# Kernel tuning notes

Hardware: AMD Instinct MI355X
Metric: run time of the kernel (lower is better)

## Reference

```python
import jax, jax.numpy as jnp
import numpy as np


def _conv(x, w, stride, dil):
    # VALID conv in NCHW / OIHW layout with rhs (kernel) dilation
    return jax.lax.conv_general_dilated(
        x, w, window_strides=stride, padding='VALID', rhs_dilation=dil,
        dimension_numbers=('NCHW', 'OIHW', 'NCHW'))


def setup_inputs() -> dict:
    key = jax.random.key(0)
    k1, k2, k3 = jax.random.split(key, 3)
    B, Cin, H, W = 8, 64, 256, 256  # W even => columns_mod2 == 0
    Cout = 128
    inp = jax.random.normal(k1, (B, Cin, H, W), dtype=jnp.float32)
    # kaiming-normal-style init as in the torch module
    fan0 = Cin * 3 * 1
    kernel0 = jax.random.normal(k2, (Cout, Cin, 3, 1), dtype=jnp.float32) * np.float32(np.sqrt(2.0 / fan0))
    fan1 = Cin * 2 * 2
    kernel1 = jax.random.normal(k3, (Cout, Cin, 2, 2), dtype=jnp.float32) * np.float32(np.sqrt(2.0 / fan1))
    bias = jnp.full((Cout,), 0.01, dtype=jnp.float32)
    return {'input': inp, 'kernel0': kernel0, 'kernel1': kernel1, 'bias': bias}


def reference(input, kernel0, kernel1, bias):
    # hexagdly conv2d, size=1, stride=1, even number of columns (columns_mod2 = 0)
    x = input
    # kernel0: vertical 3x1 stencil over all columns; bias added once here
    even_all = _conv(jnp.pad(x, ((0, 0), (0, 0), (1, 1), (0, 0))), kernel0, (1, 1), (1, 1))
    even_all = even_all + bias[None, :, None, None]
    # kernel1: 2x2 stencil with horizontal dilation 2, stride 2 in width,
    # with column-parity-dependent vertical offset (hex grid)
    # odd columns: ZeroPad2d(left=1, right=0, top=1, bottom=0)
    ooc = _conv(jnp.pad(x, ((0, 0), (0, 0), (1, 0), (1, 0))), kernel1, (1, 2), (1, 2))
    # even columns: ZeroPad2d(left=0, right=1, top=0, bottom=1)
    oec = _conv(jnp.pad(x, ((0, 0), (0, 0), (0, 1), (0, 1))), kernel1, (1, 2), (1, 2))
    # interleave columns: out[..., 2k] = ooc[..., k], out[..., 2k+1] = oec[..., k]
    B, C, H, Wh = ooc.shape
    inter = jnp.stack([ooc, oec], axis=-1).reshape(B, C, H, 2 * Wh)
    return even_all + inter
```

## Files before the change

### kernel.cpp

```cpp
#include <hip/hip_runtime.h>
#include <hip/hip_bf16.h>


#define CIN  64
#define COUT 128
#define HH   256
#define WW   256
#define TH   8
#define TW   32
#define XR   10
#define XC   34

typedef __attribute__((ext_vector_type(8))) short short8;
typedef __attribute__((ext_vector_type(4))) float f32x4;

static __device__ __forceinline__ unsigned short f2bf(float v) {
    __hip_bfloat16 h = __float2bfloat16(v);
    return __builtin_bit_cast(unsigned short, h);
}

typedef __attribute__((address_space(1))) const unsigned int asg_u32;
typedef __attribute__((address_space(3))) unsigned int asl_u32;
static __device__ __forceinline__ void gl2lds16(const void* g, void* l) {
    __builtin_amdgcn_global_load_lds((asg_u32*)g, (asl_u32*)l, 16, 0, 0);
}

#define XS_BYTES   (XR * XC * CIN * 2)
#define WTB_OFF    XS_BYTES
#define SMEM_BYTES (XS_BYTES + 2 * COUT * CIN * 2)
#define OT_STRIDE  33
#define WTAP       (COUT * CIN)

__global__ __launch_bounds__(512)
void prep_weights(const float* __restrict__ k0, const float* __restrict__ k1,
                  unsigned short* __restrict__ wsw)
{
    const int idx = blockIdx.x * 512 + threadIdx.x;
    if (idx >= 7 * COUT * 8) return;
    const int t   = idx >> 10;
    const int co  = (idx >> 3) & 127;
    const int ci0 = (idx & 7) * 8;
    short8 wv;
    #pragma unroll
    for (int j = 0; j < 8; ++j) {
        const int ci = ci0 + j;
        float v = (t < 3) ? k0[(co * CIN + ci) * 3 + t]
                          : k1[(co * CIN + ci) * 4 + (t - 3)];
        wv[j] = (short)f2bf(v);
    }
    const int e = (co * CIN + ci0) ^ ((co & 7) * 8);
    *(short8*)&wsw[t * WTAP + e] = wv;
}

__global__ __launch_bounds__(512, 4)
void hexconv_mfma(const float* __restrict__ x,
                  const unsigned short* __restrict__ wsw,
                  const float* __restrict__ bias,
                  float* __restrict__ out)
{
    __shared__ alignas(16) char smem[SMEM_BYTES];
    __shared__ float bias_lds[COUT];
    unsigned short* xs  = (unsigned short*)smem;
    unsigned short* wtb = (unsigned short*)(smem + WTB_OFF);
    float*          ot  = (float*)smem;

    const int tid  = threadIdx.x;
    const int lane = tid & 63;
    const int wid  = tid >> 6;

    const int wg = (blockIdx.x & 7) * 256 + (blockIdx.x >> 3);
    const int bx = wg & 7;
    const int by = (wg >> 3) & 31;
    const int b  = wg >> 8;

    const int h0 = by * TH;
    const int w0 = bx * TW;

    auto stage_tap = [&](int t, int buf) {
        const unsigned short* s0 = wsw + t * WTAP + wid * 1024;
        unsigned short* d0 = wtb + buf * WTAP + wid * 1024;
        gl2lds16(s0 + lane * 8, d0);
        gl2lds16(s0 + 512 + lane * 8, d0 + 512);
    };

    stage_tap(0, 0);

    if (tid < COUT) bias_lds[tid] = bias[tid];

    {
        const float* xb = x + (size_t)b * CIN * HH * WW;
        const int cg = tid & 7;
        const int u0 = tid >> 3;
        #pragma unroll
        for (int it = 0; it < 5; ++it) {
            const int u   = u0 + it * 64;
            const int row = u >> 5;
            const int ci  = (u & 31) * 2;
            const int gh  = h0 - 1 + row;
            f32x4 a = (f32x4)0.0f, c = (f32x4)0.0f;
            if ((unsigned)gh < HH) {
                const float* pb = xb + ((size_t)ci * HH + gh) * WW + w0 + 4 * cg;
                a = *(const f32x4*)pb;
                c = *(const f32x4*)(pb + HH * WW);
            }
            #pragma unroll
            for (int k = 0; k < 4; ++k) {
                const int col = 4 * cg + 1 + k;
                unsigned int pk = (unsigned int)f2bf(a[k]) | ((unsigned int)f2bf(c[k]) << 16);
                const int e = ((row * XC + col) * CIN + ci) ^ ((col & 7) * 8);
                *(unsigned int*)&xs[e] = pk;
            }
        }
        for (int i = tid; i < 2 * XR * CIN; i += 512) {
            const int side = (i >= XR * CIN) ? 1 : 0;
            const int rem  = i - side * XR * CIN;
            const int row  = rem >> 6;
            const int ci   = rem & 63;
            const int col  = side ? (XC - 1) : 0;
            const int gh   = h0 - 1 + row;
            const int gw   = side ? (w0 + TW) : (w0 - 1);
            float v = 0.f;
            if ((unsigned)gh < HH && (unsigned)gw < WW)
                v = xb[((size_t)ci * HH + gh) * WW + gw];
            const int e = ((row * XC + col) * CIN + ci) ^ ((col & 7) * 8);
            xs[e] = f2bf(v);
        }
    }

    __syncthreads();

    const int wm   = wid & 1;
    const int wn   = wid >> 1;
    const int c15  = lane & 15;
    const int q8   = (lane >> 4) * 8;
    const int par  = lane & 1;

    const int aBase = (wm * 64 + c15) * CIN + q8;
    const int swzA  = (c15 & 7) * 8;

    f32x4 acc[4][4];
    #pragma unroll
    for (int mi = 0; mi < 4; ++mi)
        #pragma unroll
        for (int ni = 0; ni < 4; ++ni)
            acc[mi][ni] = (f32x4)0.0f;

    #pragma unroll
    for (int tap = 0; tap < 7; ++tap) {
        if (tap < 6) {
            stage_tap(tap + 1, (tap + 1) & 1);
            asm volatile("s_waitcnt vmcnt(2)" ::: "memory");
        } else {
            asm volatile("s_waitcnt vmcnt(0)" ::: "memory");
        }
        __builtin_amdgcn_s_barrier();
        __builtin_amdgcn_sched_barrier(0);

        const unsigned short* wc = wtb + (tap & 1) * WTAP;

        int R0, P, C0;
        if (tap < 3) { R0 = tap; P = 0; C0 = 1; }
        else { R0 = (tap - 3) >> 1; P = 1; C0 = ((tap - 3) & 1) * 2; }
        const int colb  = c15 + C0;
        const int swzB  = (colb & 7) * 8;
        const int bBase = ((wn * 2 + R0 + P * par) * XC + colb) * CIN + q8;

        #pragma unroll
        for (int ci0 = 0; ci0 < CIN; ci0 += 32) {
            short8 af[4];
            #pragma unroll
            for (int mi = 0; mi < 4; ++mi)
                af[mi] = *(const short8*)&wc[(aBase + mi * 16 * CIN + ci0) ^ swzA];
            #pragma unroll
            for (int ni = 0; ni < 4; ++ni) {
                const int hr = ni >> 1, chalf = ni & 1;
                const int e = (bBase + hr * (XC * CIN) + chalf * (16 * CIN) + ci0) ^ swzB;
                short8 bf = *(const short8*)&xs[e];
                #pragma unroll
                for (int mi = 0; mi < 4; ++mi)
                    acc[mi][ni] = __builtin_amdgcn_mfma_f32_16x16x32_bf16(
                        af[mi], bf, acc[mi][ni], 0, 0, 0);
            }
        }

        asm volatile("s_waitcnt lgkmcnt(0)" ::: "memory");
        __builtin_amdgcn_sched_barrier(0);
        __builtin_amdgcn_s_barrier();
    }

    #pragma unroll
    for (int p = 0; p < 2; ++p) {
        if (wm == p) {
            #pragma unroll
            for (int mi = 0; mi < 4; ++mi) {
                #pragma unroll
                for (int ni = 0; ni < 4; ++ni) {
                    const int hh   = wn * 2 + (ni >> 1);
                    const int wloc = (ni & 1) * 16 + c15;
                    #pragma unroll
                    for (int r = 0; r < 4; ++r) {
                        const int col = mi * 16 + (lane >> 4) * 4 + r;
                        ot[(col * TH + hh) * OT_STRIDE + wloc] =
                            acc[mi][ni][r] + bias_lds[p * 64 + col];
                    }
                }
            }
        }
        asm volatile("s_waitcnt lgkmcnt(0)" ::: "memory");
        __builtin_amdgcn_sched_barrier(0);
        __builtin_amdgcn_s_barrier();
        #pragma unroll
        for (int it = 0; it < 8; ++it) {
            const int col = it * 8 + (tid >> 6);
            const int hh  = (tid >> 3) & 7;
            const int w4  = (tid & 7) * 4;
            const float* src = &ot[(col * TH + hh) * OT_STRIDE + w4];
            f32x4 v = { src[0], src[1], src[2], src[3] };
            __builtin_nontemporal_store(v,
                (f32x4*)&out[(((size_t)b * COUT + p * 64 + col) * HH + h0 + hh) * WW + w0 + w4]);
        }
        if (p == 0) {
            asm volatile("s_waitcnt lgkmcnt(0)" ::: "memory");
            __builtin_amdgcn_sched_barrier(0);
            __builtin_amdgcn_s_barrier();
        }
    }
}

extern "C" void kernel_launch(void* const* d_in, const int* in_sizes, int n_in,
                              void* d_out, int out_size, void* d_ws, size_t ws_size,
                              hipStream_t stream) {
    const float* x    = (const float*)d_in[0];
    const float* k0   = (const float*)d_in[1];
    const float* k1   = (const float*)d_in[2];
    const float* bias = (const float*)d_in[3];
    float* out        = (float*)d_out;
    unsigned short* wsw = (unsigned short*)d_ws;

    prep_weights<<<dim3(14, 1, 1), 512, 0, stream>>>(k0, k1, wsw);
    hexconv_mfma<<<dim3(2048, 1, 1), 512, 0, stream>>>(x, wsw, bias, out);
}
```

Measured before the change: 98.41 us.

## Read weights directly from global memory and store outputs straight from registers

Weight fragments are no longer staged into double-buffered LDS with async global-to-LDS loads and per-tap barriers; each wave loads its A fragments directly from global (L2-resident) memory. The epilogue drops the LDS transpose and writes accumulators straight to global with scalar nontemporal stores. This cuts LDS footprint and barriers, which could raise occupancy, but adds global-load latency inside the MFMA loop and replaces coalesced 16-byte stores with narrower 64-byte-segment scalar stores.

After: 164.1 us. 66.7% more time.

```diff
diff --git a/kernel.cpp b/kernel.cpp
--- a/kernel.cpp
+++ b/kernel.cpp
@@ -19,17 +19,7 @@
     return __builtin_bit_cast(unsigned short, h);
 }
 
-typedef __attribute__((address_space(1))) const unsigned int asg_u32;
-typedef __attribute__((address_space(3))) unsigned int asl_u32;
-static __device__ __forceinline__ void gl2lds16(const void* g, void* l) {
-    __builtin_amdgcn_global_load_lds((asg_u32*)g, (asl_u32*)l, 16, 0, 0);
-}
-
-#define XS_BYTES   (XR * XC * CIN * 2)
-#define WTB_OFF    XS_BYTES
-#define SMEM_BYTES (XS_BYTES + 2 * COUT * CIN * 2)
-#define OT_STRIDE  33
-#define WTAP       (COUT * CIN)
+#define WTAP (COUT * CIN)
 
 __global__ __launch_bounds__(512)
 void prep_weights(const float* __restrict__ k0, const float* __restrict__ k1,
@@ -48,8 +38,7 @@
                           : k1[(co * CIN + ci) * 4 + (t - 3)];
         wv[j] = (short)f2bf(v);
     }
-    const int e = (co * CIN + ci0) ^ ((co & 7) * 8);
-    *(short8*)&wsw[t * WTAP + e] = wv;
+    *(short8*)&wsw[t * WTAP + co * CIN + ci0] = wv;
 }
 
 __global__ __launch_bounds__(512, 4)
@@ -58,11 +47,8 @@
                   const float* __restrict__ bias,
                   float* __restrict__ out)
 {
-    __shared__ alignas(16) char smem[SMEM_BYTES];
+    __shared__ alignas(16) unsigned short xs[XR * XC * CIN];
     __shared__ float bias_lds[COUT];
-    unsigned short* xs  = (unsigned short*)smem;
-    unsigned short* wtb = (unsigned short*)(smem + WTB_OFF);
-    float*          ot  = (float*)smem;
 
     const int tid  = threadIdx.x;
     const int lane = tid & 63;
@@ -75,15 +61,6 @@
 
     const int h0 = by * TH;
     const int w0 = bx * TW;
-
-    auto stage_tap = [&](int t, int buf) {
-        const unsigned short* s0 = wsw + t * WTAP + wid * 1024;
-        unsigned short* d0 = wtb + buf * WTAP + wid * 1024;
-        gl2lds16(s0 + lane * 8, d0);
-        gl2lds16(s0 + 512 + lane * 8, d0 + 512);
-    };
-
-    stage_tap(0, 0);
 
     if (tid < COUT) bias_lds[tid] = bias[tid];
 
@@ -135,8 +112,7 @@
     const int q8   = (lane >> 4) * 8;
     const int par  = lane & 1;
 
-    const int aBase = (wm * 64 + c15) * CIN + q8;
-    const int swzA  = (c15 & 7) * 8;
+    const unsigned short* wbase = wsw + (wm * 64 + c15) * CIN + q8;
 
     f32x4 acc[4][4];
     #pragma unroll
@@ -147,17 +123,6 @@
 
     #pragma unroll
     for (int tap = 0; tap < 7; ++tap) {
-        if (tap < 6) {
-            stage_tap(tap + 1, (tap + 1) & 1);
-            asm volatile("s_waitcnt vmcnt(2)" ::: "memory");
-        } else {
-            asm volatile("s_waitcnt vmcnt(0)" ::: "memory");
-        }
-        __builtin_amdgcn_s_barrier();
-        __builtin_amdgcn_sched_barrier(0);
-
-        const unsigned short* wc = wtb + (tap & 1) * WTAP;
-
         int R0, P, C0;
         if (tap < 3) { R0 = tap; P = 0; C0 = 1; }
         else { R0 = (tap - 3) >> 1; P = 1; C0 = ((tap - 3) & 1) * 2; }
@@ -165,12 +130,14 @@
         const int swzB  = (colb & 7) * 8;
         const int bBase = ((wn * 2 + R0 + P * par) * XC + colb) * CIN + q8;
 
+        const unsigned short* wt = wbase + tap * WTAP;
+
         #pragma unroll
         for (int ci0 = 0; ci0 < CIN; ci0 += 32) {
             short8 af[4];
             #pragma unroll
             for (int mi = 0; mi < 4; ++mi)
-                af[mi] = *(const short8*)&wc[(aBase + mi * 16 * CIN + ci0) ^ swzA];
+                af[mi] = *(const short8*)&wt[mi * 16 * CIN + ci0];
             #pragma unroll
             for (int ni = 0; ni < 4; ++ni) {
                 const int hr = ni >> 1, chalf = ni & 1;
@@ -182,47 +149,23 @@
                         af[mi], bf, acc[mi][ni], 0, 0, 0);
             }
         }
-
-        asm volatile("s_waitcnt lgkmcnt(0)" ::: "memory");
-        __builtin_amdgcn_sched_barrier(0);
-        __builtin_amdgcn_s_barrier();
     }
 
     #pragma unroll
-    for (int p = 0; p < 2; ++p) {
-        if (wm == p) {
+    for (int mi = 0; mi < 4; ++mi) {
+        const int cobase = wm * 64 + mi * 16 + (lane >> 4) * 4;
+        #pragma unroll
+        for (int r = 0; r < 4; ++r) {
+            const int co = cobase + r;
+            const float bv = bias_lds[co];
+            float* orow = out + ((size_t)b * COUT + co) * HH * WW;
             #pragma unroll
-            for (int mi = 0; mi < 4; ++mi) {
-                #pragma unroll
-                for (int ni = 0; ni < 4; ++ni) {
-                    const int hh   = wn * 2 + (ni >> 1);
-                    const int wloc = (ni & 1) * 16 + c15;
-                    #pragma unroll
-                    for (int r = 0; r < 4; ++r) {
-                        const int col = mi * 16 + (lane >> 4) * 4 + r;
-                        ot[(col * TH + hh) * OT_STRIDE + wloc] =
-                            acc[mi][ni][r] + bias_lds[p * 64 + col];
-                    }
-                }
+            for (int ni = 0; ni < 4; ++ni) {
+                const int h = h0 + wn * 2 + (ni >> 1);
+                const int w = w0 + (ni & 1) * 16 + c15;
+                __builtin_nontemporal_store(acc[mi][ni][r] + bv,
+                                            &orow[(size_t)h * WW + w]);
             }
-        }
-        asm volatile("s_waitcnt lgkmcnt(0)" ::: "memory");
-        __builtin_amdgcn_sched_barrier(0);
-        __builtin_amdgcn_s_barrier();
-        #pragma unroll
-        for (int it = 0; it < 8; ++it) {
-            const int col = it * 8 + (tid >> 6);
-            const int hh  = (tid >> 3) & 7;
-            const int w4  = (tid & 7) * 4;
-            const float* src = &ot[(col * TH + hh) * OT_STRIDE + w4];
-            f32x4 v = { src[0], src[1], src[2], src[3] };
-            __builtin_nontemporal_store(v,
-                (f32x4*)&out[(((size_t)b * COUT + p * 64 + col) * HH + h0 + hh) * WW + w0 + w4]);
-        }
-        if (p == 0) {
-            asm volatile("s_waitcnt lgkmcnt(0)" ::: "memory");
-            __builtin_amdgcn_sched_barrier(0);
-            __builtin_amdgcn_s_barrier();
         }
     }
 }
```
